# Performance work log

Measured on AMD Instinct MI355X. Metric: run time of the kernel, lower is better.

Reference implementation:

```python
import jax, jax.numpy as jnp
import numpy as np

QMIN, QMAX = -128.0, 127.0


def fake_quantize(x, scale, zero_point):
    # quantize->dequantize (int8 cast in torch only clips; values already integral)
    q = jnp.clip(jnp.round(x / scale) + zero_point, QMIN, QMAX)
    return (q - zero_point) * scale


def _bk_resolvent_diag(he_diag, h0_super, h0_sub, z):
    """Diagonal of G = (z - H)^{-1} for tridiagonal H via two continued-fraction sweeps.
    he_diag: (B, N) float32; h0_super/h0_sub: (N-1,) float32; z: complex scalar.
    Returns (B, N) complex64.
    """
    a = he_diag.astype(jnp.complex64).T          # (N, B)
    c = (h0_sub * h0_super).astype(jnp.complex64)  # (N-1,) coupling b_i * c_i
    Bsz = a.shape[1]
    zero = jnp.zeros((Bsz,), jnp.complex64)

    def step(carry, inp):
        ai, ci = inp
        new = ci / (z - ai - carry)
        return new, new

    # Left sweep: L_0 = 0, L_i = c_{i-1} / (z - a_{i-1} - L_{i-1})
    _, Lrest = jax.lax.scan(step, zero, (a[:-1], c))
    L = jnp.concatenate([zero[None], Lrest], axis=0)          # (N, B)
    # Right sweep: R_{N-1} = 0, R_i = c_i / (z - a_{i+1} - R_{i+1})
    _, Rrest = jax.lax.scan(step, zero, (a[1:][::-1], c[::-1]))
    R = jnp.concatenate([zero[None], Rrest], axis=0)[::-1]     # (N, B)

    G = 1.0 / (z - a - L - R)                                   # (N, B)
    return G.T


def setup_inputs() -> dict:
    key = jax.random.key(0)
    B, N = 512, 16384
    v_fp32 = jax.random.normal(key, (B, N), dtype=jnp.float32)
    h0_diag = jnp.full((N,), -2.0, dtype=jnp.float32)
    h0_sub = jnp.ones((N - 1,), dtype=jnp.float32)
    h0_super = jnp.ones((N - 1,), dtype=jnp.float32)
    return {"v_fp32": v_fp32, "h0_diag": h0_diag, "h0_sub": h0_sub, "h0_super": h0_super}


def reference(v_fp32, h0_diag, h0_sub, h0_super):
    # fake-quantize the potential (training path, scale=1.0, zp=0 defaults)
    v = fake_quantize(v_fp32, jnp.float32(1.0), jnp.float32(0.0))
    he_diag = jnp.clip(h0_diag[None, :] + v, -10.0, 10.0)       # (B, N)
    z = jnp.complex64(1j)
    G = _bk_resolvent_diag(he_diag, h0_super, h0_sub, z)        # (B, N) complex
    G_real = jnp.clip(G.real.astype(jnp.float32), -100.0, 100.0)
    G_imag = jnp.clip(G.imag.astype(jnp.float32), -100.0, 100.0)
    G_real = fake_quantize(G_real, jnp.float32(1.0), jnp.float32(0.0))
    G_imag = fake_quantize(G_imag, jnp.float32(1.0), jnp.float32(0.0))
    return jnp.stack([G_real, G_imag], axis=-1)                 # (B, N, 2)
```

## Files before the change

### kernel.cpp

```cpp
#include <hip/hip_runtime.h>


#define SEG   32
#define WARM  32
#define LANES 64
#define CHUNK (LANES*SEG)
#define HALO  WARM
#define STAGE (CHUNK + 2*HALO)
#define SPAD  (STAGE + STAGE/32 + 1)

struct C2 { float r, i; };

__device__ __forceinline__ int padi(int i) { return i + (i >> 5); }

__device__ __forceinline__ C2 npdiv(float nr, float dr, float di) {
  #pragma clang fp contract(off)
  const bool  b   = fabsf(dr) >= fabsf(di);
  const float num = b ? di : dr;
  const float den = b ? dr : di;
  const float rat = num / den;
  const float t   = num * rat;
  const float s   = den + t;
  const float scl = 1.0f / s;
  const float u   = nr * scl;
  const float m   = nr * rat;
  const float w   = m * scl;
  C2 o;
  o.r = b ? u : w;
  o.i = b ? -w : -u;
  return o;
}

__device__ __forceinline__ void cf_step(float na, float cv, float& cr, float& ci) {
  #pragma clang fp contract(off)
  const float dr = na - cr;
  const float di = 1.0f - ci;
  const C2 nc = npdiv(cv, dr, di);
  cr = nc.r; ci = nc.i;
}

__device__ __forceinline__ float neg_a(float vv, float hd) {
  #pragma clang fp contract(off)
  float q = rintf(vv);
  q = fminf(fmaxf(q, -128.0f), 127.0f);
  float he = hd + q;
  he = fminf(fmaxf(he, -10.0f), 10.0f);
  return 0.0f - he;
}

__device__ __forceinline__ float fq_out(float x) {
  #pragma clang fp contract(off)
  x = fminf(fmaxf(x, -100.0f), 100.0f);
  x = rintf(x);
  x = fminf(fmaxf(x, -128.0f), 127.0f);
  return x;
}

__global__ void cc_kernel(const float* __restrict__ hsub,
                          const float* __restrict__ hsup,
                          float* __restrict__ ccf, int N) {
  #pragma clang fp contract(off)
  const int i = blockIdx.x * blockDim.x + threadIdx.x;
  if (i < N + 2*HALO + 8) {
    const int k = i - HALO;
    ccf[i] = (k >= 0 && k < N - 1) ? hsub[k] * hsup[k] : 0.0f;
  }
}

__device__ __forceinline__ void load8_f(const float4* __restrict__ cc4,
                                        int m0, float* w) {
  const int q = (m0 + HALO) >> 2;
  const float4 A = cc4[q];
  const float4 B = cc4[q + 1];
  w[0]=A.x; w[1]=A.y; w[2]=A.z; w[3]=A.w;
  w[4]=B.x; w[5]=B.y; w[6]=B.z; w[7]=B.w;
}

__device__ __forceinline__ void load8_b(const float4* __restrict__ cc4,
                                        int m0, float* w) {
  const int q = (m0 + HALO - 3) >> 2;
  const float4 A = cc4[q];
  const float4 B = cc4[q + 1];
  const float4 C = cc4[q + 2];
  w[0]=A.w;
  w[1]=B.x; w[2]=B.y; w[3]=B.z; w[4]=B.w;
  w[5]=C.x; w[6]=C.y; w[7]=C.z;
}

__global__ void __launch_bounds__(LANES, 4)
bk_kernel(const float* __restrict__ v,
          const float* __restrict__ hdiag,
          const float* __restrict__ ccf,
          float2* __restrict__ out,
          int N, int chunks_per_row) {
  #pragma clang fp contract(off)
  __shared__ float sA[SPAD];

  const int tid  = threadIdx.x;
  const int row  = blockIdx.x / chunks_per_row;
  const int ch   = blockIdx.x - row * chunks_per_row;
  const int base = ch * CHUNK;
  const long rowoff = (long)row * N;
  const float4* cc4 = (const float4*)ccf;

  for (int i = tid; i < STAGE; i += LANES) {
    const int k = base - HALO + i;
    float na = 0.0f;
    if (k >= 0 && k < N) na = neg_a(v[rowoff + k], hdiag[k]);
    sA[padi(i)] = na;
  }
  __syncthreads();

  const int s0  = base + tid * SEG;
  const int s1  = s0 + SEG;
  const int li0 = tid * SEG + HALO;

  float Rr[SEG], Ri[SEG];
  float cr, ci, wc[8];

  cr = 0.0f; ci = 0.0f;
  for (int g = 0; g < WARM / 8; ++g) {
    const int kh = s1 + (WARM - 1) - 8 * g;
    load8_b(cc4, kh - 8, wc);
    #pragma unroll
    for (int j = 0; j < 8; ++j) {
      const float na = sA[padi(kh - j - base + HALO)];
      cf_step(na, wc[7 - j], cr, ci);
    }
  }
  Rr[SEG-1] = cr; Ri[SEG-1] = ci;

  #pragma unroll
  for (int tg = 0; tg < SEG / 8; ++tg) {
    const int th = SEG - 1 - 8 * tg;
    load8_b(cc4, s0 + th - 8, wc);
    #pragma unroll
    for (int j = 0; j < 8; ++j) {
      const int t = th - j;
      if (t >= 1) {
        const float na = sA[padi(li0 + t)];
        cf_step(na, wc[7 - j], cr, ci);
        Rr[t-1] = cr; Ri[t-1] = ci;
      }
    }
  }

  cr = 0.0f; ci = 0.0f;
  for (int g = 0; g < WARM / 8; ++g) {
    const int kl = s0 - WARM + 8 * g;
    load8_f(cc4, kl, wc);
    #pragma unroll
    for (int j = 0; j < 8; ++j) {
      const float na = sA[padi(kl + j - base + HALO)];
      cf_step(na, wc[j], cr, ci);
    }
  }

  #pragma unroll
  for (int tg = 0; tg < SEG / 8; ++tg) {
    const int kl = s0 + 8 * tg;
    load8_f(cc4, kl, wc);
    #pragma unroll
    for (int j = 0; j < 8; ++j) {
      const int t = 8 * tg + j;
      const float na  = sA[padi(li0 + t)];
      const float drL = na - cr;
      const float diL = 1.0f - ci;
      const float drf = drL - Rr[t];
      const float dif = diL - Ri[t];
      const C2 G = npdiv(1.0f, drf, dif);
      out[rowoff + kl + j] = make_float2(fq_out(G.r), fq_out(G.i));
      if (t < SEG - 1) {
        const C2 nc = npdiv(wc[j], drL, diL);
        cr = nc.r; ci = nc.i;
      }
    }
  }
}

extern "C" void kernel_launch(void* const* d_in, const int* in_sizes, int n_in,
                              void* d_out, int out_size, void* d_ws, size_t ws_size,
                              hipStream_t stream) {
  const float* v    = (const float*)d_in[0];
  const float* hd   = (const float*)d_in[1];
  const float* hsub = (const float*)d_in[2];
  const float* hsup = (const float*)d_in[3];
  const int N = in_sizes[1];
  const int B = in_sizes[0] / N;
  const int chunks = (N + CHUNK - 1) / CHUNK;

  float* ccf = (float*)d_ws;
  const int ccn = N + 2*HALO + 8;
  cc_kernel<<<(ccn + 255) / 256, 256, 0, stream>>>(hsub, hsup, ccf, N);
  bk_kernel<<<B * chunks, LANES, 0, stream>>>(v, hd, ccf, (float2*)d_out,
                                              N, chunks);
}
```

Measured before the change: 142.7 us.

## Process two interleaved segments per thread and shorten warmup halo

Each thread now handles two independent 32-element segments (A and B), so a block covers 128 segments and the two continued-fraction recurrences are interleaved. The independent chains are meant to hide the latency of the serial division sweeps through instruction-level parallelism. The warm-up length drops from 32 to 24, cutting redundant halo work, with some risk to accuracy of the truncated recurrence. Register pressure roughly doubles, since there are four 32-entry arrays per thread, which may cause spills or lower occupancy.

Measured after the change: 155.9 us. +9.3%, slower.

```diff
diff --git a/kernel.cpp b/kernel.cpp
--- a/kernel.cpp
+++ b/kernel.cpp
@@ -2,9 +2,10 @@
 
 
 #define SEG   32
-#define WARM  32
+#define WARM  24
 #define LANES 64
-#define CHUNK (LANES*SEG)
+#define NSEG  128
+#define CHUNK (NSEG*SEG)
 #define HALO  WARM
 #define STAGE (CHUNK + 2*HALO)
 #define SPAD  (STAGE + STAGE/32 + 1)
@@ -111,68 +112,102 @@
   }
   __syncthreads();
 
-  const int s0  = base + tid * SEG;
-  const int s1  = s0 + SEG;
-  const int li0 = tid * SEG + HALO;
-
-  float Rr[SEG], Ri[SEG];
-  float cr, ci, wc[8];
-
-  cr = 0.0f; ci = 0.0f;
+  const int s0A = base + tid * SEG;
+  const int s0B = s0A + 64 * SEG;
+  const int s1A = s0A + SEG;
+  const int s1B = s0B + SEG;
+  const int liA = tid * SEG + HALO;
+  const int liB = liA + 64 * SEG;
+
+  float RrA[SEG], RiA[SEG], RrB[SEG], RiB[SEG];
+  float crA, ciA, crB, ciB;
+  float wcA[8], wcB[8];
+
+  crA = 0.0f; ciA = 0.0f; crB = 0.0f; ciB = 0.0f;
   for (int g = 0; g < WARM / 8; ++g) {
-    const int kh = s1 + (WARM - 1) - 8 * g;
-    load8_b(cc4, kh - 8, wc);
-    #pragma unroll
-    for (int j = 0; j < 8; ++j) {
-      const float na = sA[padi(kh - j - base + HALO)];
-      cf_step(na, wc[7 - j], cr, ci);
-    }
-  }
-  Rr[SEG-1] = cr; Ri[SEG-1] = ci;
+    const int khA = s1A + (WARM - 1) - 8 * g;
+    const int khB = s1B + (WARM - 1) - 8 * g;
+    load8_b(cc4, khA - 8, wcA);
+    load8_b(cc4, khB - 8, wcB);
+    #pragma unroll
+    for (int j = 0; j < 8; ++j) {
+      const float naA = sA[padi(khA - j - base + HALO)];
+      const float naB = sA[padi(khB - j - base + HALO)];
+      cf_step(naA, wcA[7 - j], crA, ciA);
+      cf_step(naB, wcB[7 - j], crB, ciB);
+    }
+  }
+  RrA[SEG-1] = crA; RiA[SEG-1] = ciA;
+  RrB[SEG-1] = crB; RiB[SEG-1] = ciB;
 
   #pragma unroll
   for (int tg = 0; tg < SEG / 8; ++tg) {
     const int th = SEG - 1 - 8 * tg;
-    load8_b(cc4, s0 + th - 8, wc);
+    load8_b(cc4, s0A + th - 8, wcA);
+    load8_b(cc4, s0B + th - 8, wcB);
     #pragma unroll
     for (int j = 0; j < 8; ++j) {
       const int t = th - j;
       if (t >= 1) {
-        const float na = sA[padi(li0 + t)];
-        cf_step(na, wc[7 - j], cr, ci);
-        Rr[t-1] = cr; Ri[t-1] = ci;
+        const float naA = sA[padi(liA + t)];
+        const float naB = sA[padi(liB + t)];
+        cf_step(naA, wcA[7 - j], crA, ciA);
+        cf_step(naB, wcB[7 - j], crB, ciB);
+        RrA[t-1] = crA; RiA[t-1] = ciA;
+        RrB[t-1] = crB; RiB[t-1] = ciB;
       }
     }
   }
 
-  cr = 0.0f; ci = 0.0f;
+  crA = 0.0f; ciA = 0.0f; crB = 0.0f; ciB = 0.0f;
   for (int g = 0; g < WARM / 8; ++g) {
-    const int kl = s0 - WARM + 8 * g;
-    load8_f(cc4, kl, wc);
-    #pragma unroll
-    for (int j = 0; j < 8; ++j) {
-      const float na = sA[padi(kl + j - base + HALO)];
-      cf_step(na, wc[j], cr, ci);
+    const int klA = s0A - WARM + 8 * g;
+    const int klB = s0B - WARM + 8 * g;
+    load8_f(cc4, klA, wcA);
+    load8_f(cc4, klB, wcB);
+    #pragma unroll
+    for (int j = 0; j < 8; ++j) {
+      const float naA = sA[padi(klA + j - base + HALO)];
+      const float naB = sA[padi(klB + j - base + HALO)];
+      cf_step(naA, wcA[j], crA, ciA);
+      cf_step(naB, wcB[j], crB, ciB);
     }
   }
 
   #pragma unroll
   for (int tg = 0; tg < SEG / 8; ++tg) {
-    const int kl = s0 + 8 * tg;
-    load8_f(cc4, kl, wc);
+    const int klA = s0A + 8 * tg;
+    const int klB = s0B + 8 * tg;
+    load8_f(cc4, klA, wcA);
+    load8_f(cc4, klB, wcB);
     #pragma unroll
     for (int j = 0; j < 8; ++j) {
       const int t = 8 * tg + j;
-      const float na  = sA[padi(li0 + t)];
-      const float drL = na - cr;
-      const float diL = 1.0f - ci;
-      const float drf = drL - Rr[t];
-      const float dif = diL - Ri[t];
-      const C2 G = npdiv(1.0f, drf, dif);
-      out[rowoff + kl + j] = make_float2(fq_out(G.r), fq_out(G.i));
-      if (t < SEG - 1) {
-        const C2 nc = npdiv(wc[j], drL, diL);
-        cr = nc.r; ci = nc.i;
+      {
+        const float na  = sA[padi(liA + t)];
+        const float drL = na - crA;
+        const float diL = 1.0f - ciA;
+        const float drf = drL - RrA[t];
+        const float dif = diL - RiA[t];
+        const C2 G = npdiv(1.0f, drf, dif);
+        out[rowoff + klA + j] = make_float2(fq_out(G.r), fq_out(G.i));
+        if (t < SEG - 1) {
+          const C2 nc = npdiv(wcA[j], drL, diL);
+          crA = nc.r; ciA = nc.i;
+        }
+      }
+      {
+        const float na  = sA[padi(liB + t)];
+        const float drL = na - crB;
+        const float diL = 1.0f - ciB;
+        const float drf = drL - RrB[t];
+        const float dif = diL - RiB[t];
+        const C2 G = npdiv(1.0f, drf, dif);
+        out[rowoff + klB + j] = make_float2(fq_out(G.r), fq_out(G.i));
+        if (t < SEG - 1) {
+          const C2 nc = npdiv(wcB[j], drL, diL);
+          crB = nc.r; ciB = nc.i;
+        }
       }
     }
   }
```
